# Performance work log

Measured on AMD Instinct MI355X. Metric: run time of the kernel, lower is better.

## Reference

```python
import jax, jax.numpy as jnp
import numpy as np

B, A, F, D, C = 256, 128, 512, 6, 512  # batch, max_atoms, atom_features, max_degree, conv_width


def setup_inputs() -> dict:
    key = jax.random.key(0)
    k1, k2, k3, k4 = jax.random.split(key, 4)
    atoms = jax.random.normal(k1, (B, A, F), dtype=jnp.float32)
    # neighbour indices in [0, A); pad entries beyond each atom's degree with -1
    neigh = jax.random.randint(k2, (B, A, D), 0, A)
    deg = jax.random.randint(k3, (B, A, 1), 0, D)  # degrees in 0..D-1
    bonds = jnp.where(jnp.arange(D)[None, None, :] < deg, neigh, -1)
    # one Dense(conv_width) per degree: stacked kernels [D, F, C] and biases [D, C]
    W = jax.random.normal(k4, (D, F, C), dtype=jnp.float32) * 0.02
    b = jnp.zeros((D, C), dtype=jnp.float32)
    return {"atoms": atoms, "bonds": bonds, "W": W, "b": b}


def reference(atoms, bonds, W, b):
    d_max = bonds.shape[-1]
    # per-atom degree = count of non -1 neighbour slots  [B, A, 1]
    degrees = jnp.sum(bonds != -1, axis=-1, keepdims=True)
    # shift lookup by 1 so that padded (-1) neighbours index a zero row
    padded = jnp.pad(atoms, ((0, 0), (1, 1), (0, 0)))  # [B, A+2, F]
    idx = bonds + 1  # [B, A, D]
    # per-sample gather of neighbour features -> [B, A, D, F]
    neigh_feats = jax.vmap(lambda ref, i: ref[i])(padded, idx)
    summed = jnp.sum(neigh_feats, axis=2) + atoms  # [B, A, F]
    # apply all degree-specific dense layers, then mask-select by degree
    dense = jnp.einsum('baf,dfc->badc', summed, W) + b  # [B, A, D, C]
    masks = (degrees[..., None] == jnp.arange(d_max).reshape(1, 1, d_max, 1)).astype(dense.dtype)
    return jnp.sum(dense * masks, axis=2)  # [B, A, C]
```

## Files before the change

kernel.cpp:

```cpp
#include <hip/hip_runtime.h>
#include <hip/hip_bf16.h>


#define NB 256
#define NA 128
#define NF 512
#define ND 6
#define NC 512
#define NATOMS (NB * NA)

#define NT_TRANS 1536
#define NT_BUCK  32

typedef __attribute__((ext_vector_type(8))) short frag8;
typedef __attribute__((ext_vector_type(4))) float f32x4;

static __device__ inline unsigned short f2bu(float f) {
    __hip_bfloat16 h = __float2bfloat16(f);
    return *reinterpret_cast<unsigned short*>(&h);
}
static __device__ inline unsigned int pack2(float a, float b) {
    return (unsigned int)f2bu(a) | ((unsigned int)f2bu(b) << 16);
}
static __device__ inline float b2f(unsigned short u) {
    __hip_bfloat16 h;
    *reinterpret_cast<unsigned short*>(&h) = u;
    return __bfloat162float(h);
}
static __device__ inline void async16(const void* g, void* l) {
    __builtin_amdgcn_global_load_lds(
        (const __attribute__((address_space(1))) void*)g,
        (__attribute__((address_space(3))) void*)l, 16, 0, 0);
}

__global__ __launch_bounds__(256) void prep_misc(
    const float* __restrict__ W, __hip_bfloat16* __restrict__ Wt,
    const int* __restrict__ bonds, int* __restrict__ counts,
    int* __restrict__ bucket) {
    const int bid = blockIdx.x;
    const int tid = threadIdx.x;
    __shared__ float t[32][33];
    __shared__ int lcnt[ND];
    __shared__ int lbase[ND];

    if (bid < NT_TRANS) {
        const int tx = tid & 31, ty = tid >> 5;
        const int c0 = (bid & 15) * 32;
        const int f0 = ((bid >> 4) & 15) * 32;
        const int d  = bid >> 8;
        #pragma unroll
        for (int r = 0; r < 32; r += 8)
            t[ty + r][tx] =
                W[((size_t)(d * NF + f0 + ty + r)) * NC + c0 + tx];
        __syncthreads();
        #pragma unroll
        for (int r = 0; r < 32; r += 8)
            Wt[((size_t)(d * NC + c0 + ty + r)) * NF + f0 + tx] =
                __float2bfloat16(t[tx][ty + r]);
        return;
    }
    const int b = bid - NT_TRANS;
    if (tid < ND) lcnt[tid] = 0;
    __syncthreads();
    int deg[4], loc[4], gg[4];
    #pragma unroll
    for (int i = 0; i < 4; ++i) {
        int g = b * 1024 + i * 256 + tid;
        gg[i] = g;
        int dg = 0;
        #pragma unroll
        for (int j = 0; j < ND; ++j) dg += (bonds[g * ND + j] >= 0);
        deg[i] = dg;
        loc[i] = atomicAdd(&lcnt[dg], 1);
    }
    __syncthreads();
    if (tid < ND) lbase[tid] = atomicAdd(&counts[tid], lcnt[tid]);
    __syncthreads();
    #pragma unroll
    for (int i = 0; i < 4; ++i)
        bucket[deg[i] * NATOMS + lbase[deg[i]] + loc[i]] = gg[i];
}

__global__ __launch_bounds__(512, 2) void sum_mol(
    const float* __restrict__ atoms, const int* __restrict__ bonds,
    __hip_bfloat16* __restrict__ summed) {
    __shared__ __align__(16) __hip_bfloat16 mol[NA * NF];
    char* molB = (char*)mol;
    const int m   = blockIdx.x;
    const int tid = threadIdx.x;

    const float4* a4 = (const float4*)atoms + (size_t)m * (NA * NF / 4);
    #pragma unroll 4
    for (int i = 0; i < 32; ++i) {
        float4 v = a4[i * 512 + tid];
        const int r  = i * 4 + (tid >> 7);
        const int co = tid & 127;
        uint2 pk; pk.x = pack2(v.x, v.y); pk.y = pack2(v.z, v.w);
        *(uint2*)(molB + r * 1024 + (((co >> 1) ^ (r & 7)) << 4) + (co & 1) * 8) = pk;
    }
    __syncthreads();

    const int a  = tid >> 2;
    const int qd = tid & 3;
    const int* bd = bonds + (size_t)(m * NA + a) * ND;
    int   nb[ND], x7[ND];
    float msk[ND];
    #pragma unroll
    for (int j = 0; j < ND; ++j) {
        int n = bd[j];
        msk[j] = (n >= 0) ? 1.0f : 0.0f;
        nb[j]  = (n >= 0) ? n : 0;
        x7[j]  = nb[j] & 7;
    }
    const int a7 = a & 7;
    char* outB = (char*)summed + (size_t)(m * NA + a) * 1024;

    #pragma unroll 4
    for (int ci = 0; ci < 16; ++ci) {
        const int c = qd * 16 + ci;
        const frag8 s = *(const frag8*)(molB + a * 1024 + ((c ^ a7) << 4));
        float acc[8];
        #pragma unroll
        for (int e = 0; e < 8; ++e) acc[e] = b2f((unsigned short)s[e]);
        #pragma unroll
        for (int j = 0; j < ND; ++j) {
            const frag8 v = *(const frag8*)(molB + nb[j] * 1024 + ((c ^ x7[j]) << 4));
            #pragma unroll
            for (int e = 0; e < 8; ++e)
                acc[e] = fmaf(b2f((unsigned short)v[e]), msk[j], acc[e]);
        }
        uint4 o;
        o.x = pack2(acc[0], acc[1]); o.y = pack2(acc[2], acc[3]);
        o.z = pack2(acc[4], acc[5]); o.w = pack2(acc[6], acc[7]);
        *(uint4*)(outB + c * 16) = o;
    }
}

__global__ __launch_bounds__(512, 4) void gemm_deg(
    const __hip_bfloat16* __restrict__ summed, const __hip_bfloat16* __restrict__ Wt,
    const float* __restrict__ bias, const int* __restrict__ counts,
    const int* __restrict__ bucket, float* __restrict__ out) {
    const int L  = blockIdx.x + 24 * blockIdx.y;
    const int q  = L >> 3;
    const int p  = ((q >> 1) << 3) + (L & 7);
    const int d  = p % ND;
    const int m0 = (p / ND) * 128;
    const int n0 = (q & 1) * 256;
    const int Md = counts[d];
    if (m0 >= Md) return;

    __shared__ __align__(16) __hip_bfloat16 sA[3][128 * 32];
    __shared__ __align__(16) __hip_bfloat16 sB[3][256 * 32];
    __shared__ int sRows[128];

    const int tid = threadIdx.x;
    if (tid < 128) {
        int r = m0 + tid;
        sRows[tid] = (r < Md) ? bucket[d * NATOMS + r] : -1;
    }
    __syncthreads();

    const int lane = tid & 63;
    const int w    = tid >> 6;

    const int sr = lane >> 2;
    const int sl = lane & 3;
    const int gseg = sl ^ ((sr >> 1) & 3);

    const int rA = w * 16 + sr;
    const char* smB = (const char*)summed;
    const char* wtB = (const char*)Wt + (size_t)(d * NC + n0) * 1024;
    int g0 = sRows[rA];
    const size_t gA0 = (size_t)((g0 < 0) ? 0 : g0) * 1024;
    const size_t gB0 = (size_t)(w * 16 + sr) * 1024;
    const size_t gB1 = (size_t)(128 + w * 16 + sr) * 1024;

    const int quad = lane >> 4, l16 = lane & 15;
    const int xr2  = (l16 >> 1) & 3;
    const int wy = w >> 2, wx = w & 3;

    f32x4 acc[4][4];
    #pragma unroll
    for (int i = 0; i < 4; ++i)
        #pragma unroll
        for (int j = 0; j < 4; ++j) acc[i][j] = (f32x4)0.0f;

    auto stage = [&](int buf, int kt) {
        const int koff = kt * 64 + gseg * 16;
        async16(smB + gA0 + koff, (char*)&sA[buf][0] + w * 1024);
        async16(wtB + gB0 + koff, (char*)&sB[buf][0] + w * 1024);
        async16(wtB + gB1 + koff, (char*)&sB[buf][0] + 8192 + w * 1024);
    };
    auto compute = [&](int buf) {
        frag8 aF[4], bF[4];
        #pragma unroll
        for (int i = 0; i < 4; ++i)
            aF[i] = *(const frag8*)&sA[buf][(wy * 64 + i * 16 + l16) * 32 +
                                            ((quad ^ xr2) << 3)];
        #pragma unroll
        for (int j = 0; j < 4; ++j)
            bF[j] = *(const frag8*)&sB[buf][(wx * 64 + j * 16 + l16) * 32 +
                                            ((quad ^ xr2) << 3)];
        #pragma unroll
        for (int i = 0; i < 4; ++i)
            #pragma unroll
            for (int j = 0; j < 4; ++j)
                acc[i][j] = __builtin_amdgcn_mfma_f32_16x16x32_bf16(
                    aF[i], bF[j], acc[i][j], 0, 0, 0);
    };

    stage(0, 0);
    stage(1, 1);
    #pragma unroll
    for (int kt = 0; kt < NF / 32; ++kt) {
        if (kt < NF / 32 - 1)
            asm volatile("s_waitcnt vmcnt(3)" ::: "memory");
        else
            asm volatile("s_waitcnt vmcnt(0)" ::: "memory");
        __builtin_amdgcn_sched_barrier(0);
        __builtin_amdgcn_s_barrier();
        if (kt + 2 < NF / 32) stage((kt + 2) % 3, kt + 2);
        __builtin_amdgcn_s_setprio(1);
        compute(kt % 3);
        __builtin_amdgcn_s_setprio(0);
    }

    float bv[4];
    #pragma unroll
    for (int j = 0; j < 4; ++j)
        bv[j] = bias[d * NC + n0 + wx * 64 + j * 16 + l16];
    #pragma unroll
    for (int i = 0; i < 4; ++i) {
        #pragma unroll
        for (int r = 0; r < 4; ++r) {
            const int tr = wy * 64 + i * 16 + quad * 4 + r;
            const int g  = sRows[tr];
            if (g < 0) continue;
            float* orow = out + (size_t)g * NC + n0 + wx * 64 + l16;
            #pragma unroll
            for (int j = 0; j < 4; ++j)
                __builtin_nontemporal_store(acc[i][j][r] + bv[j], orow + j * 16);
        }
    }
}

extern "C" void kernel_launch(void* const* d_in, const int* in_sizes, int n_in,
                              void* d_out, int out_size, void* d_ws, size_t ws_size,
                              hipStream_t stream) {
    const float* atoms = (const float*)d_in[0];
    const int*   bonds = (const int*)d_in[1];
    const float* W     = (const float*)d_in[2];
    const float* bias  = (const float*)d_in[3];
    float* out = (float*)d_out;

    char* ws = (char*)d_ws;
    int* counts = (int*)ws;
    int* bucket = (int*)(ws + 1024);
    __hip_bfloat16* Wt     = (__hip_bfloat16*)(ws + 1024 + 786432);
    __hip_bfloat16* summed = (__hip_bfloat16*)(ws + 1024 + 786432 + 3145728);

    hipMemsetAsync(counts, 0, 1024, stream);

    prep_misc<<<NT_TRANS + NT_BUCK, 256, 0, stream>>>(W, Wt, bonds, counts, bucket);

    sum_mol<<<NB, 512, 0, stream>>>(atoms, bonds, summed);

    gemm_deg<<<dim3(24, 128), 512, 0, stream>>>(
        summed, Wt, bias, counts, bucket, out);
}
```

Measured before the change: 171.9 us.

## Stage summed and GEMM epilogue through LDS for coalesced vector global stores

The neighbour-sum kernel now holds its packed results in registers, writes them back into the swizzled LDS tile, and then copies whole rows out with contiguous 16-byte stores instead of per-thread scattered row writes. The degree GEMM epilogue stages its accumulators in reused shared memory, two halves at a time, so each output row is written as coalesced float4 nontemporal stores with a vector bias add, replacing scalar strided stores. This targets global write efficiency at the cost of extra barriers and LDS traffic, plus higher register pressure from the 16-entry psum array.

```diff
diff --git a/kernel.cpp b/kernel.cpp
--- a/kernel.cpp
+++ b/kernel.cpp
@@ -14,6 +14,7 @@
 
 typedef __attribute__((ext_vector_type(8))) short frag8;
 typedef __attribute__((ext_vector_type(4))) float f32x4;
+typedef __attribute__((ext_vector_type(4))) unsigned int u32x4;
 
 static __device__ inline unsigned short f2bu(float f) {
     __hip_bfloat16 h = __float2bfloat16(f);
@@ -113,9 +114,9 @@
         x7[j]  = nb[j] & 7;
     }
     const int a7 = a & 7;
-    char* outB = (char*)summed + (size_t)(m * NA + a) * 1024;
-
-    #pragma unroll 4
+
+    u32x4 psum[16];
+    #pragma unroll
     for (int ci = 0; ci < 16; ++ci) {
         const int c = qd * 16 + ci;
         const frag8 s = *(const frag8*)(molB + a * 1024 + ((c ^ a7) << 4));
@@ -129,10 +130,27 @@
             for (int e = 0; e < 8; ++e)
                 acc[e] = fmaf(b2f((unsigned short)v[e]), msk[j], acc[e]);
         }
-        uint4 o;
-        o.x = pack2(acc[0], acc[1]); o.y = pack2(acc[2], acc[3]);
-        o.z = pack2(acc[4], acc[5]); o.w = pack2(acc[6], acc[7]);
-        *(uint4*)(outB + c * 16) = o;
+        u32x4 o;
+        o[0] = pack2(acc[0], acc[1]); o[1] = pack2(acc[2], acc[3]);
+        o[2] = pack2(acc[4], acc[5]); o[3] = pack2(acc[6], acc[7]);
+        psum[ci] = o;
+    }
+
+    __syncthreads();
+    #pragma unroll
+    for (int ci = 0; ci < 16; ++ci) {
+        const int c = qd * 16 + ci;
+        *(u32x4*)(molB + a * 1024 + ((c ^ a7) << 4)) = psum[ci];
+    }
+    __syncthreads();
+
+    const int chunk = tid & 63;
+    char* dst = (char*)summed + (size_t)m * (NA * NF * 2);
+    #pragma unroll
+    for (int t = 0; t < 16; ++t) {
+        const int row = t * 8 + (tid >> 6);
+        u32x4 v = *(const u32x4*)(molB + row * 1024 + ((chunk ^ (row & 7)) << 4));
+        *(u32x4*)(dst + row * 1024 + chunk * 16) = v;
     }
 }
 
@@ -149,9 +167,10 @@
     const int Md = counts[d];
     if (m0 >= Md) return;
 
-    __shared__ __align__(16) __hip_bfloat16 sA[3][128 * 32];
-    __shared__ __align__(16) __hip_bfloat16 sB[3][256 * 32];
-    __shared__ int sRows[128];
+    __shared__ __align__(16) char smem[74240];
+    char* const sAb   = smem;
+    char* const sBb   = smem + 24576;
+    int*  const sRows = (int*)(smem + 73728);
 
     const int tid = threadIdx.x;
     if (tid < 128) {
@@ -167,10 +186,9 @@
     const int sl = lane & 3;
     const int gseg = sl ^ ((sr >> 1) & 3);
 
-    const int rA = w * 16 + sr;
     const char* smB = (const char*)summed;
     const char* wtB = (const char*)Wt + (size_t)(d * NC + n0) * 1024;
-    int g0 = sRows[rA];
+    int g0 = sRows[w * 16 + sr];
     const size_t gA0 = (size_t)((g0 < 0) ? 0 : g0) * 1024;
     const size_t gB0 = (size_t)(w * 16 + sr) * 1024;
     const size_t gB1 = (size_t)(128 + w * 16 + sr) * 1024;
@@ -187,20 +205,22 @@
 
     auto stage = [&](int buf, int kt) {
         const int koff = kt * 64 + gseg * 16;
-        async16(smB + gA0 + koff, (char*)&sA[buf][0] + w * 1024);
-        async16(wtB + gB0 + koff, (char*)&sB[buf][0] + w * 1024);
-        async16(wtB + gB1 + koff, (char*)&sB[buf][0] + 8192 + w * 1024);
+        async16(smB + gA0 + koff, sAb + buf * 8192 + w * 1024);
+        async16(wtB + gB0 + koff, sBb + buf * 16384 + w * 1024);
+        async16(wtB + gB1 + koff, sBb + buf * 16384 + 8192 + w * 1024);
     };
     auto compute = [&](int buf) {
+        const __hip_bfloat16* A  = (const __hip_bfloat16*)(sAb + buf * 8192);
+        const __hip_bfloat16* Bm = (const __hip_bfloat16*)(sBb + buf * 16384);
         frag8 aF[4], bF[4];
         #pragma unroll
         for (int i = 0; i < 4; ++i)
-            aF[i] = *(const frag8*)&sA[buf][(wy * 64 + i * 16 + l16) * 32 +
-                                            ((quad ^ xr2) << 3)];
+            aF[i] = *(const frag8*)&A[(wy * 64 + i * 16 + l16) * 32 +
+                                      ((quad ^ xr2) << 3)];
         #pragma unroll
         for (int j = 0; j < 4; ++j)
-            bF[j] = *(const frag8*)&sB[buf][(wx * 64 + j * 16 + l16) * 32 +
-                                            ((quad ^ xr2) << 3)];
+            bF[j] = *(const frag8*)&Bm[(wx * 64 + j * 16 + l16) * 32 +
+                                       ((quad ^ xr2) << 3)];
         #pragma unroll
         for (int i = 0; i < 4; ++i)
             #pragma unroll
@@ -225,21 +245,34 @@
         __builtin_amdgcn_s_setprio(0);
     }
 
-    float bv[4];
-    #pragma unroll
-    for (int j = 0; j < 4; ++j)
-        bv[j] = bias[d * NC + n0 + wx * 64 + j * 16 + l16];
-    #pragma unroll
-    for (int i = 0; i < 4; ++i) {
-        #pragma unroll
-        for (int r = 0; r < 4; ++r) {
-            const int tr = wy * 64 + i * 16 + quad * 4 + r;
-            const int g  = sRows[tr];
-            if (g < 0) continue;
-            float* orow = out + (size_t)g * NC + n0 + wx * 64 + l16;
+    const int chunk = tid & 63;
+    const f32x4 bv = *(const f32x4*)&bias[d * NC + n0 + chunk * 4];
+    float* cs = (float*)smem;
+
+    #pragma unroll
+    for (int s = 0; s < 2; ++s) {
+        __syncthreads();
+        if (wy == s) {
             #pragma unroll
-            for (int j = 0; j < 4; ++j)
-                __builtin_nontemporal_store(acc[i][j][r] + bv[j], orow + j * 16);
+            for (int i = 0; i < 4; ++i)
+                #pragma unroll
+                for (int j = 0; j < 4; ++j)
+                    #pragma unroll
+                    for (int r = 0; r < 4; ++r)
+                        cs[(i * 16 + quad * 4 + r) * 256 + wx * 64 + j * 16 + l16] =
+                            acc[i][j][r];
+        }
+        __syncthreads();
+        #pragma unroll
+        for (int t = 0; t < 8; ++t) {
+            const int row = t * 8 + (tid >> 6);
+            const int g   = sRows[s * 64 + row];
+            if (g >= 0) {
+                f32x4 v = *(const f32x4*)&cs[row * 256 + chunk * 4];
+                v += bv;
+                __builtin_nontemporal_store(
+                    v, (f32x4*)(out + (size_t)g * NC + n0 + chunk * 4));
+            }
         }
     }
 }
```

Measured after the change: 166.6 us. 3.0% less time.
